# Performance work log

Measured on AMD Instinct MI355X. Metric: run time of the kernel, lower is better.

## Reference

```python
import jax, jax.numpy as jnp
import numpy as np

B, R, S = 4, 16384, 96

def setup_inputs() -> dict:
    key = jax.random.key(0)
    k1, k2, k3, k4 = jax.random.split(key, 4)
    colors = jax.random.normal(k1, (B, R, S, 3), dtype=jnp.float32)
    densities = jax.random.normal(k2, (B, R, S, 1), dtype=jnp.float32)
    # depths must be monotonically increasing along the sample axis
    depths = jnp.sort(jax.random.uniform(k3, (B, R, S, 1), dtype=jnp.float32), axis=2)
    sample_coordinates = jax.random.uniform(k4, (B, R, S, 3), dtype=jnp.float32)
    return {"colors": colors, "densities": densities, "depths": depths,
            "sample_coordinates": sample_coordinates, "white_back": 0}


def reference(colors, densities, depths, sample_coordinates, white_back):
    deltas = depths[:, :, 1:] - depths[:, :, :-1]                     # [B,R,S-1,1]
    colors_mid = (colors[:, :, :-1] + colors[:, :, 1:]) * 0.5
    densities_mid = (densities[:, :, :-1] + densities[:, :, 1:]) * 0.5
    depths_mid = (depths[:, :, :-1] + depths[:, :, 1:]) * 0.5
    coords_mid = (sample_coordinates[:, :, :-1] + sample_coordinates[:, :, 1:]) * 0.5

    densities_mid = jax.nn.softplus(densities_mid)                    # activation_factory
    alpha = 1.0 - jnp.exp(-densities_mid * deltas)                    # [B,R,S-1,1]

    ones = jnp.ones_like(alpha[:, :, :1])
    alpha_shifted = jnp.concatenate([ones, 1.0 - alpha + 1e-10], axis=-2)
    trans = jnp.cumprod(alpha_shifted, axis=-2)[:, :, :-1]            # transmittance T_i

    weights = alpha * trans                                            # [B,R,S-1,1]
    tau = trans[:, :, -1, :]                                           # [B,R,1]

    composite_rgb = jnp.sum(weights * colors_mid, axis=-2)             # [B,R,3]
    composite_point = jnp.sum(weights * coords_mid, axis=-2)           # [B,R,3]
    weight_total = jnp.sum(weights, axis=2)                            # [B,R,1]

    composite_depth = jnp.sum(weights * depths_mid, axis=-2)           # [B,R,1]
    composite_depth = jnp.nan_to_num(composite_depth, nan=jnp.inf)
    composite_depth = jnp.clip(composite_depth, jnp.min(depths), jnp.max(depths))

    composite_rgb = jnp.where(white_back != 0,
                              composite_rgb + 1.0 - weight_total,
                              composite_rgb)
    return composite_rgb, composite_depth, weights, composite_point, tau
```

## Files before the change

kernel.cpp:

```cpp
#include <hip/hip_runtime.h>

#define NRAYS 65536
#define NS    96
#define NI    95

#define OFF_RGB   0
#define OFF_DEPTH 196608
#define OFF_W     262144
#define OFF_PT    6488064
#define OFF_TAU   6684672

__global__ void depth_minmax_sorted(const float* __restrict__ deps, unsigned* ws) {
    const int t = blockIdx.x * blockDim.x + threadIdx.x;
    float lo = deps[(size_t)t * NS];
    float hi = deps[(size_t)t * NS + (NS - 1)];
    #pragma unroll
    for (int off = 32; off; off >>= 1) {
        lo = fminf(lo, __shfl_xor(lo, off, 64));
        hi = fmaxf(hi, __shfl_xor(hi, off, 64));
    }
    if ((threadIdx.x & 63) == 0) {
        atomicMin(&ws[0], __float_as_uint(lo));
        atomicMin(&ws[1], ~__float_as_uint(hi));
    }
}

__device__ __forceinline__ float softplus_fast(float x) {
    return fmaxf(x, 0.0f) + __logf(1.0f + __expf(-fabsf(x)));
}

__device__ __forceinline__ void gload_lds16(const float* gp, float* lp) {
    __builtin_amdgcn_global_load_lds(
        (const __attribute__((address_space(1))) void*)gp,
        (__attribute__((address_space(3))) void*)lp,
        16, 0, 0);
}

__launch_bounds__(256, 4)
__global__ void raymarch(const float* __restrict__ colors,
                         const float* __restrict__ dens,
                         const float* __restrict__ deps,
                         const float* __restrict__ coords,
                         const int* __restrict__ wbp,
                         const unsigned* __restrict__ mm,
                         float* __restrict__ out) {
    __shared__ float sbuf[4 * 2304];

    const int tid  = threadIdx.x;
    const int lane = tid & 63;
    const int wv   = tid >> 6;
    const int sub  = lane & 15;
    const int r4   = lane >> 4;
    const int g    = blockIdx.x * 16 + wv * 4 + r4;
    const size_t rb0 = (size_t)blockIdx.x * 16 + wv * 4;

    const float2* dq = (const float2*)(deps + (size_t)g * NS + 6 * sub);
    const float2* nq = (const float2*)(dens + (size_t)g * NS + 6 * sub);
    float2 dv0 = dq[0], dv1 = dq[1], dv2 = dq[2];
    float2 nv0 = nq[0], nv1 = nq[1], nv2 = nq[2];

    __builtin_amdgcn_sched_barrier(0);

    float* cl = sbuf + wv * 2304;
    float* pl = cl + 1152;
    {
        const float* cg = colors + rb0 * (NS * 3);
        const float* pg = coords + rb0 * (NS * 3);
        #pragma unroll
        for (int k = 0; k < 4; ++k) gload_lds16(cg + 4 * lane + 256 * k, cl + 256 * k);
        #pragma unroll
        for (int k = 0; k < 4; ++k) gload_lds16(pg + 4 * lane + 256 * k, pl + 256 * k);
        if (lane < 32) {
            gload_lds16(cg + 1024 + 4 * lane, cl + 1024);
            gload_lds16(pg + 1024 + 4 * lane, pl + 1024);
        }
    }

    float d[6], n[6];
    d[0] = dv0.x; d[1] = dv0.y; d[2] = dv1.x; d[3] = dv1.y; d[4] = dv2.x; d[5] = dv2.y;
    n[0] = nv0.x; n[1] = nv0.y; n[2] = nv1.x; n[3] = nv1.y; n[4] = nv2.x; n[5] = nv2.y;
    const int nsrc = (lane & 48) | ((sub + 1) & 15);
    float d6 = __shfl(d[0], nsrc, 64);
    float n6 = __shfl(n[0], nsrc, 64);

    float a[6], f[6];
    #pragma unroll
    for (int i = 0; i < 6; ++i) {
        float dn1 = (i < 5) ? d[i+1] : d6;
        float nn1 = (i < 5) ? n[i+1] : n6;
        float E = __expf(-softplus_fast(0.5f * (n[i] + nn1)) * (dn1 - d[i]));
        const bool valid = (i < 5) || (sub < 15);
        a[i] = valid ? (1.0f - E) : 0.0f;
        f[i] = valid ? (E + 1e-10f) : 1.0f;
    }

    float incl = ((f[0] * f[1]) * (f[2] * f[3])) * (f[4] * f[5]);
    #pragma unroll
    for (int off = 1; off < 16; off <<= 1) {
        float t = __shfl_up(incl, off, 16);
        if (sub >= off) incl *= t;
    }
    float excl = __shfl_up(incl, 1, 16);
    if (sub == 0) excl = 1.0f;

    asm volatile("s_waitcnt vmcnt(0)" ::: "memory");

    float c[18], p[18], cn0, cn1, cn2, pn0, pn1, pn2;
    {
        const float2* qc = (const float2*)(cl + r4 * 288 + 18 * sub);
        const float2* qp = (const float2*)(pl + r4 * 288 + 18 * sub);
        #pragma unroll
        for (int j = 0; j < 9; ++j) { float2 v = qc[j]; c[2*j] = v.x; c[2*j+1] = v.y; }
        #pragma unroll
        for (int j = 0; j < 9; ++j) { float2 v = qp[j]; p[2*j] = v.x; p[2*j+1] = v.y; }
        const int noff = (sub < 15) ? 18 * (sub + 1) : 0;
        cn0 = cl[r4 * 288 + noff + 0];
        cn1 = cl[r4 * 288 + noff + 1];
        cn2 = cl[r4 * 288 + noff + 2];
        pn0 = pl[r4 * 288 + noff + 0];
        pn1 = pl[r4 * 288 + noff + 1];
        pn2 = pl[r4 * 288 + noff + 2];
    }

    float acc[8];
    #pragma unroll
    for (int k = 0; k < 8; ++k) acc[k] = 0.0f;
    float t = excl;
    float tauc = 0.0f;
    const size_t wb = (size_t)OFF_W + (size_t)g * NI + 6 * sub;
    #pragma unroll
    for (int i = 0; i < 6; ++i) {
        float w = a[i] * t;
        if (i < 5 || sub < 15) out[wb + i] = w;
        float dn1 = (i < 5) ? d[i+1] : d6;
        float dm  = 0.5f * (d[i] + dn1);
        float cmx = 0.5f * (c[3*i+0] + ((i < 5) ? c[3*i+3] : cn0));
        float cmy = 0.5f * (c[3*i+1] + ((i < 5) ? c[3*i+4] : cn1));
        float cmz = 0.5f * (c[3*i+2] + ((i < 5) ? c[3*i+5] : cn2));
        float pmx = 0.5f * (p[3*i+0] + ((i < 5) ? p[3*i+3] : pn0));
        float pmy = 0.5f * (p[3*i+1] + ((i < 5) ? p[3*i+4] : pn1));
        float pmz = 0.5f * (p[3*i+2] + ((i < 5) ? p[3*i+5] : pn2));
        acc[0] += w * cmx;  acc[1] += w * cmy;  acc[2] += w * cmz;
        acc[3] += w * pmx;  acc[4] += w * pmy;  acc[5] += w * pmz;
        acc[6] += w * dm;   acc[7] += w;
        if (i == 4) tauc = t;
        t *= f[i];
    }
    float tau = __shfl(tauc, (lane & 48) | 15, 64);

    #pragma unroll
    for (int k = 0; k < 8; ++k) {
        #pragma unroll
        for (int off = 1; off < 16; off <<= 1)
            acc[k] += __shfl_xor(acc[k], off, 64);
    }

    if (sub == 0) {
        float add = (wbp != nullptr && wbp[0] != 0) ? (1.0f - acc[7]) : 0.0f;
        size_t rb = (size_t)OFF_RGB + (size_t)g * 3;
        out[rb + 0] = acc[0] + add;
        out[rb + 1] = acc[1] + add;
        out[rb + 2] = acc[2] + add;
        size_t pb = (size_t)OFF_PT + (size_t)g * 3;
        out[pb + 0] = acc[3];
        out[pb + 1] = acc[4];
        out[pb + 2] = acc[5];
        float cd = acc[6];
        if (cd != cd) cd = __int_as_float(0x7f800000);
        float dmin = __uint_as_float(mm[0]);
        float dmax = __uint_as_float(~mm[1]);
        cd = fminf(fmaxf(cd, dmin), dmax);
        out[OFF_DEPTH + g] = cd;
        out[OFF_TAU + g]   = tau;
    }
}

extern "C" void kernel_launch(void* const* d_in, const int* in_sizes, int n_in,
                              void* d_out, int out_size, void* d_ws, size_t ws_size,
                              hipStream_t stream) {
    const float* colors = (const float*)d_in[0];
    const float* dens   = (const float*)d_in[1];
    const float* deps   = (const float*)d_in[2];
    const float* coords = (const float*)d_in[3];
    const int*   wb     = (n_in > 4) ? (const int*)d_in[4] : nullptr;
    float* out = (float*)d_out;
    unsigned* mm = (unsigned*)d_ws;

    hipMemsetAsync(mm, 0xFF, 8, stream);
    depth_minmax_sorted<<<NRAYS / 256, 256, 0, stream>>>(deps, mm);
    raymarch<<<NRAYS / 16, 256, 0, stream>>>(colors, dens, deps, coords, wb, mm, out);
}
```

Before: 236.9 us.

## Make raymarch persistent with double-buffered LDS DMA of all inputs

The raymarch kernel now launches 256 blocks, one per CU, instead of one block per 16 rays. Each wave loops over 16 groups of 4 rays and double-buffers colors, coords, depths and densities into LDS with global_load_lds, prefetching two groups ahead. The goal is to overlap memory fetch with compute and to cut launch and tail overhead. In exchange, occupancy drops to 4 waves per CU with only two groups in flight per wave, which may not be enough outstanding memory traffic to saturate HBM. The vmcnt-based waits also count the stores issued in earlier iterations.

```diff
diff --git a/kernel.cpp b/kernel.cpp
--- a/kernel.cpp
+++ b/kernel.cpp
@@ -36,7 +36,31 @@
         16, 0, 0);
 }
 
-__launch_bounds__(256, 4)
+__device__ __forceinline__ void issue_dma(const float* __restrict__ colors,
+                                          const float* __restrict__ coords,
+                                          const float* __restrict__ deps,
+                                          const float* __restrict__ dens,
+                                          int grp, float* lbuf, int lane) {
+    const size_t rb0 = (size_t)grp * 4;
+    const float* cg = colors + rb0 * (NS * 3);
+    const float* pg = coords + rb0 * (NS * 3);
+    const float* dg = deps   + rb0 * NS;
+    const float* ng = dens   + rb0 * NS;
+    #pragma unroll
+    for (int k = 0; k < 4; ++k) gload_lds16(cg + 4 * lane + 256 * k, lbuf + 256 * k);
+    #pragma unroll
+    for (int k = 0; k < 4; ++k) gload_lds16(pg + 4 * lane + 256 * k, lbuf + 1152 + 256 * k);
+    gload_lds16(dg + 4 * lane, lbuf + 2304);
+    gload_lds16(ng + 4 * lane, lbuf + 2688);
+    if (lane < 32) {
+        gload_lds16(cg + 1024 + 4 * lane, lbuf + 1024);
+        gload_lds16(pg + 1024 + 4 * lane, lbuf + 1152 + 1024);
+        gload_lds16(dg +  256 + 4 * lane, lbuf + 2304 + 256);
+        gload_lds16(ng +  256 + 4 * lane, lbuf + 2688 + 256);
+    }
+}
+
+__launch_bounds__(256, 1)
 __global__ void raymarch(const float* __restrict__ colors,
                          const float* __restrict__ dens,
                          const float* __restrict__ deps,
@@ -44,134 +68,135 @@
                          const int* __restrict__ wbp,
                          const unsigned* __restrict__ mm,
                          float* __restrict__ out) {
-    __shared__ float sbuf[4 * 2304];
+    __shared__ float sbuf[4 * 2 * 3072];
 
     const int tid  = threadIdx.x;
     const int lane = tid & 63;
     const int wv   = tid >> 6;
     const int sub  = lane & 15;
     const int r4   = lane >> 4;
-    const int g    = blockIdx.x * 16 + wv * 4 + r4;
-    const size_t rb0 = (size_t)blockIdx.x * 16 + wv * 4;
-
-    const float2* dq = (const float2*)(deps + (size_t)g * NS + 6 * sub);
-    const float2* nq = (const float2*)(dens + (size_t)g * NS + 6 * sub);
-    float2 dv0 = dq[0], dv1 = dq[1], dv2 = dq[2];
-    float2 nv0 = nq[0], nv1 = nq[1], nv2 = nq[2];
-
-    __builtin_amdgcn_sched_barrier(0);
-
-    float* cl = sbuf + wv * 2304;
-    float* pl = cl + 1152;
-    {
-        const float* cg = colors + rb0 * (NS * 3);
-        const float* pg = coords + rb0 * (NS * 3);
-        #pragma unroll
-        for (int k = 0; k < 4; ++k) gload_lds16(cg + 4 * lane + 256 * k, cl + 256 * k);
-        #pragma unroll
-        for (int k = 0; k < 4; ++k) gload_lds16(pg + 4 * lane + 256 * k, pl + 256 * k);
-        if (lane < 32) {
-            gload_lds16(cg + 1024 + 4 * lane, cl + 1024);
-            gload_lds16(pg + 1024 + 4 * lane, pl + 1024);
-        }
-    }
-
-    float d[6], n[6];
-    d[0] = dv0.x; d[1] = dv0.y; d[2] = dv1.x; d[3] = dv1.y; d[4] = dv2.x; d[5] = dv2.y;
-    n[0] = nv0.x; n[1] = nv0.y; n[2] = nv1.x; n[3] = nv1.y; n[4] = nv2.x; n[5] = nv2.y;
-    const int nsrc = (lane & 48) | ((sub + 1) & 15);
-    float d6 = __shfl(d[0], nsrc, 64);
-    float n6 = __shfl(n[0], nsrc, 64);
-
-    float a[6], f[6];
-    #pragma unroll
-    for (int i = 0; i < 6; ++i) {
-        float dn1 = (i < 5) ? d[i+1] : d6;
-        float nn1 = (i < 5) ? n[i+1] : n6;
-        float E = __expf(-softplus_fast(0.5f * (n[i] + nn1)) * (dn1 - d[i]));
-        const bool valid = (i < 5) || (sub < 15);
-        a[i] = valid ? (1.0f - E) : 0.0f;
-        f[i] = valid ? (E + 1e-10f) : 1.0f;
-    }
-
-    float incl = ((f[0] * f[1]) * (f[2] * f[3])) * (f[4] * f[5]);
-    #pragma unroll
-    for (int off = 1; off < 16; off <<= 1) {
-        float t = __shfl_up(incl, off, 16);
-        if (sub >= off) incl *= t;
-    }
-    float excl = __shfl_up(incl, 1, 16);
-    if (sub == 0) excl = 1.0f;
-
-    asm volatile("s_waitcnt vmcnt(0)" ::: "memory");
-
-    float c[18], p[18], cn0, cn1, cn2, pn0, pn1, pn2;
-    {
-        const float2* qc = (const float2*)(cl + r4 * 288 + 18 * sub);
-        const float2* qp = (const float2*)(pl + r4 * 288 + 18 * sub);
-        #pragma unroll
-        for (int j = 0; j < 9; ++j) { float2 v = qc[j]; c[2*j] = v.x; c[2*j+1] = v.y; }
-        #pragma unroll
-        for (int j = 0; j < 9; ++j) { float2 v = qp[j]; p[2*j] = v.x; p[2*j+1] = v.y; }
-        const int noff = (sub < 15) ? 18 * (sub + 1) : 0;
-        cn0 = cl[r4 * 288 + noff + 0];
-        cn1 = cl[r4 * 288 + noff + 1];
-        cn2 = cl[r4 * 288 + noff + 2];
-        pn0 = pl[r4 * 288 + noff + 0];
-        pn1 = pl[r4 * 288 + noff + 1];
-        pn2 = pl[r4 * 288 + noff + 2];
-    }
-
-    float acc[8];
-    #pragma unroll
-    for (int k = 0; k < 8; ++k) acc[k] = 0.0f;
-    float t = excl;
-    float tauc = 0.0f;
-    const size_t wb = (size_t)OFF_W + (size_t)g * NI + 6 * sub;
-    #pragma unroll
-    for (int i = 0; i < 6; ++i) {
-        float w = a[i] * t;
-        if (i < 5 || sub < 15) out[wb + i] = w;
-        float dn1 = (i < 5) ? d[i+1] : d6;
-        float dm  = 0.5f * (d[i] + dn1);
-        float cmx = 0.5f * (c[3*i+0] + ((i < 5) ? c[3*i+3] : cn0));
-        float cmy = 0.5f * (c[3*i+1] + ((i < 5) ? c[3*i+4] : cn1));
-        float cmz = 0.5f * (c[3*i+2] + ((i < 5) ? c[3*i+5] : cn2));
-        float pmx = 0.5f * (p[3*i+0] + ((i < 5) ? p[3*i+3] : pn0));
-        float pmy = 0.5f * (p[3*i+1] + ((i < 5) ? p[3*i+4] : pn1));
-        float pmz = 0.5f * (p[3*i+2] + ((i < 5) ? p[3*i+5] : pn2));
-        acc[0] += w * cmx;  acc[1] += w * cmy;  acc[2] += w * cmz;
-        acc[3] += w * pmx;  acc[4] += w * pmy;  acc[5] += w * pmz;
-        acc[6] += w * dm;   acc[7] += w;
-        if (i == 4) tauc = t;
-        t *= f[i];
-    }
-    float tau = __shfl(tauc, (lane & 48) | 15, 64);
-
-    #pragma unroll
-    for (int k = 0; k < 8; ++k) {
-        #pragma unroll
-        for (int off = 1; off < 16; off <<= 1)
-            acc[k] += __shfl_xor(acc[k], off, 64);
-    }
-
-    if (sub == 0) {
-        float add = (wbp != nullptr && wbp[0] != 0) ? (1.0f - acc[7]) : 0.0f;
-        size_t rb = (size_t)OFF_RGB + (size_t)g * 3;
-        out[rb + 0] = acc[0] + add;
-        out[rb + 1] = acc[1] + add;
-        out[rb + 2] = acc[2] + add;
-        size_t pb = (size_t)OFF_PT + (size_t)g * 3;
-        out[pb + 0] = acc[3];
-        out[pb + 1] = acc[4];
-        out[pb + 2] = acc[5];
-        float cd = acc[6];
-        if (cd != cd) cd = __int_as_float(0x7f800000);
-        float dmin = __uint_as_float(mm[0]);
-        float dmax = __uint_as_float(~mm[1]);
-        cd = fminf(fmaxf(cd, dmin), dmax);
-        out[OFF_DEPTH + g] = cd;
-        out[OFF_TAU + g]   = tau;
+    const int gbase = blockIdx.x * 64;
+
+    float* wreg = sbuf + wv * 6144;
+
+    issue_dma(colors, coords, deps, dens, gbase + 0 * 4 + wv, wreg,        lane);
+    issue_dma(colors, coords, deps, dens, gbase + 1 * 4 + wv, wreg + 3072, lane);
+
+    for (int it = 0; it < 16; ++it) {
+        float* lb = wreg + (it & 1) * 3072;
+
+        if (it < 15) asm volatile("s_waitcnt vmcnt(14)" ::: "memory");
+        else         asm volatile("s_waitcnt vmcnt(0)"  ::: "memory");
+        __builtin_amdgcn_sched_barrier(0);
+
+        const int grp = gbase + it * 4 + wv;
+        const int g   = grp * 4 + r4;
+
+        float d[6], n[6], d6, n6;
+        {
+            const float2* qd = (const float2*)(lb + 2304 + r4 * 96 + 6 * sub);
+            const float2* qn = (const float2*)(lb + 2688 + r4 * 96 + 6 * sub);
+            #pragma unroll
+            for (int j = 0; j < 3; ++j) { float2 v = qd[j]; d[2*j] = v.x; d[2*j+1] = v.y; }
+            #pragma unroll
+            for (int j = 0; j < 3; ++j) { float2 v = qn[j]; n[2*j] = v.x; n[2*j+1] = v.y; }
+            const int noff = (sub < 15) ? 6 * (sub + 1) : 0;
+            d6 = lb[2304 + r4 * 96 + noff];
+            n6 = lb[2688 + r4 * 96 + noff];
+        }
+        float c[18], p[18], cn0, cn1, cn2, pn0, pn1, pn2;
+        {
+            const float2* qc = (const float2*)(lb + r4 * 288 + 18 * sub);
+            const float2* qp = (const float2*)(lb + 1152 + r4 * 288 + 18 * sub);
+            #pragma unroll
+            for (int j = 0; j < 9; ++j) { float2 v = qc[j]; c[2*j] = v.x; c[2*j+1] = v.y; }
+            #pragma unroll
+            for (int j = 0; j < 9; ++j) { float2 v = qp[j]; p[2*j] = v.x; p[2*j+1] = v.y; }
+            const int noff = (sub < 15) ? 18 * (sub + 1) : 0;
+            cn0 = lb[r4 * 288 + noff + 0];
+            cn1 = lb[r4 * 288 + noff + 1];
+            cn2 = lb[r4 * 288 + noff + 2];
+            pn0 = lb[1152 + r4 * 288 + noff + 0];
+            pn1 = lb[1152 + r4 * 288 + noff + 1];
+            pn2 = lb[1152 + r4 * 288 + noff + 2];
+        }
+
+        float a[6], f[6];
+        #pragma unroll
+        for (int i = 0; i < 6; ++i) {
+            float dn1 = (i < 5) ? d[i+1] : d6;
+            float nn1 = (i < 5) ? n[i+1] : n6;
+            float E = __expf(-softplus_fast(0.5f * (n[i] + nn1)) * (dn1 - d[i]));
+            const bool valid = (i < 5) || (sub < 15);
+            a[i] = valid ? (1.0f - E) : 0.0f;
+            f[i] = valid ? (E + 1e-10f) : 1.0f;
+        }
+
+        float incl = ((f[0] * f[1]) * (f[2] * f[3])) * (f[4] * f[5]);
+        #pragma unroll
+        for (int off = 1; off < 16; off <<= 1) {
+            float t = __shfl_up(incl, off, 16);
+            if (sub >= off) incl *= t;
+        }
+        float excl = __shfl_up(incl, 1, 16);
+        if (sub == 0) excl = 1.0f;
+
+        float acc[8];
+        #pragma unroll
+        for (int k = 0; k < 8; ++k) acc[k] = 0.0f;
+        float t = excl;
+        float tauc = 0.0f;
+        const size_t wb = (size_t)OFF_W + (size_t)g * NI + 6 * sub;
+        #pragma unroll
+        for (int i = 0; i < 6; ++i) {
+            float w = a[i] * t;
+            if (i < 5 || sub < 15) out[wb + i] = w;
+            float dn1 = (i < 5) ? d[i+1] : d6;
+            float dm  = 0.5f * (d[i] + dn1);
+            float cmx = 0.5f * (c[3*i+0] + ((i < 5) ? c[3*i+3] : cn0));
+            float cmy = 0.5f * (c[3*i+1] + ((i < 5) ? c[3*i+4] : cn1));
+            float cmz = 0.5f * (c[3*i+2] + ((i < 5) ? c[3*i+5] : cn2));
+            float pmx = 0.5f * (p[3*i+0] + ((i < 5) ? p[3*i+3] : pn0));
+            float pmy = 0.5f * (p[3*i+1] + ((i < 5) ? p[3*i+4] : pn1));
+            float pmz = 0.5f * (p[3*i+2] + ((i < 5) ? p[3*i+5] : pn2));
+            acc[0] += w * cmx;  acc[1] += w * cmy;  acc[2] += w * cmz;
+            acc[3] += w * pmx;  acc[4] += w * pmy;  acc[5] += w * pmz;
+            acc[6] += w * dm;   acc[7] += w;
+            if (i == 4) tauc = t;
+            t *= f[i];
+        }
+        float tau = __shfl(tauc, (lane & 48) | 15, 64);
+
+        #pragma unroll
+        for (int k = 0; k < 8; ++k) {
+            #pragma unroll
+            for (int off = 1; off < 16; off <<= 1)
+                acc[k] += __shfl_xor(acc[k], off, 64);
+        }
+
+        if (sub == 0) {
+            float add = (wbp != nullptr && wbp[0] != 0) ? (1.0f - acc[7]) : 0.0f;
+            size_t rb = (size_t)OFF_RGB + (size_t)g * 3;
+            out[rb + 0] = acc[0] + add;
+            out[rb + 1] = acc[1] + add;
+            out[rb + 2] = acc[2] + add;
+            size_t pb = (size_t)OFF_PT + (size_t)g * 3;
+            out[pb + 0] = acc[3];
+            out[pb + 1] = acc[4];
+            out[pb + 2] = acc[5];
+            float cd = acc[6];
+            if (cd != cd) cd = __int_as_float(0x7f800000);
+            float dmin = __uint_as_float(mm[0]);
+            float dmax = __uint_as_float(~mm[1]);
+            cd = fminf(fmaxf(cd, dmin), dmax);
+            out[OFF_DEPTH + g] = cd;
+            out[OFF_TAU + g]   = tau;
+        }
+
+        if (it < 14) {
+            __builtin_amdgcn_sched_barrier(0);
+            issue_dma(colors, coords, deps, dens, gbase + (it + 2) * 4 + wv, lb, lane);
+        }
     }
 }
 
@@ -188,5 +213,5 @@
 
     hipMemsetAsync(mm, 0xFF, 8, stream);
     depth_minmax_sorted<<<NRAYS / 256, 256, 0, stream>>>(deps, mm);
-    raymarch<<<NRAYS / 16, 256, 0, stream>>>(colors, dens, deps, coords, wb, mm, out);
-}
+    raymarch<<<256, 256, 0, stream>>>(colors, dens, deps, coords, wb, mm, out);
+}
```

Result: slower. 248.4 us (+4.8%).
